# Kernel tuning notes

Measured on AMD Instinct MI355X. Metric: run time of the kernel, lower is better.

## Reference

```python
import jax, jax.numpy as jnp
import numpy as np

N = 100000      # num nodes
E = 1000000     # num directed edges
D_IN = 128      # input feature dim
D_H = 32        # hidden dim


def setup_inputs() -> dict:
    key = jax.random.key(0)
    ks = jax.random.split(key, 10)
    feat = jax.random.normal(ks[0], (N, D_IN), jnp.float32)
    src = jax.random.randint(ks[1], (E,), 0, N, dtype=jnp.int64)
    dst = jax.random.randint(ks[2], (E,), 0, N, dtype=jnp.int64)

    def lin(k, fan_in, fan_out):
        bound = 1.0 / np.sqrt(fan_in)
        kw, kb = jax.random.split(k)
        W = jax.random.uniform(kw, (fan_in, fan_out), jnp.float32, -bound, bound)
        b = jax.random.uniform(kb, (fan_out,), jnp.float32, -bound, bound)
        return W, b

    W_in, b_in = lin(ks[3], D_IN, D_H)        # input_project
    W_nbr, b_nbr = lin(ks[4], D_H, D_H)       # W_neighbor1 (Linear incl. its own bias)
    b_neighbor1 = jnp.zeros((D_H,), jnp.float32)  # extra learned bias, zero-init
    W_ffnn, b_ffnn = lin(ks[5], 2 * D_H, D_H)
    return {"feat": feat, "src": src, "dst": dst,
            "W_in": W_in, "b_in": b_in,
            "W_nbr": W_nbr, "b_nbr": b_nbr, "b_neighbor1": b_neighbor1,
            "W_ffnn": W_ffnn, "b_ffnn": b_ffnn}


def reference(feat, src, dst, W_in, b_in, W_nbr, b_nbr, b_neighbor1, W_ffnn, b_ffnn):
    # h = input_project(feat)  (input_dim != hidden_dim)
    h = feat @ W_in + b_in                                   # [N, D_H]

    # neighbors of v = predecessors (src where dst==v) + successors (dst where src==v)
    seg = jnp.concatenate([dst, src])                        # [2E] receiving node
    nbr = jnp.concatenate([src, dst])                        # [2E] neighbor node

    # sigmoid(W_neighbor1(h[nbr]) + b_neighbor1), then per-node max-pool
    t = jax.nn.sigmoid(h[nbr] @ W_nbr + b_nbr + b_neighbor1)  # [2E, D_H]
    agg = jax.ops.segment_max(t, seg, num_segments=N)         # [N, D_H]

    # nodes with total neighbor count <= 1 get zeros (faithful to `if len > 1`)
    deg = jax.ops.segment_sum(jnp.ones_like(seg, dtype=jnp.int32), seg, num_segments=N)
    agg = jnp.where((deg > 1)[:, None], agg, jnp.zeros((), jnp.float32))

    # concat + final linear
    out = jnp.concatenate([h, agg], axis=1) @ W_ffnn + b_ffnn  # [N, D_H]
    return out
```

## Files before the change

kernel.cpp:

```cpp
#include <hip/hip_runtime.h>
#include <hip/hip_bf16.h>

#define DH 32
#define BSZ 128
#define NBP 1024
#define SCAT_E 3840
#define SCAT_P (2 * SCAT_E)
#define EPT 15
#define PRE_E 8192
#define CPG 16
#define TS 4096
#define PAD 17
#define TPW 2

typedef short bf16x8 __attribute__((ext_vector_type(8)));
typedef float f32x4 __attribute__((ext_vector_type(4)));

__device__ __forceinline__ unsigned short f2bf(float x) {
    unsigned b = __float_as_uint(x);
    b += 0x7FFFu + ((b >> 16) & 1u);
    return (unsigned short)(b >> 16);
}

__global__ __launch_bounds__(256) void pre2(
    const int* __restrict__ src, const int* __restrict__ dst,
    int* __restrict__ gtotal, int E, int pgrid,
    const float* __restrict__ W_in, const float* __restrict__ W_nbr,
    const float* __restrict__ W_ffnn, unsigned short* __restrict__ wbf)
{
    __shared__ int hist[NBP];
    const int tid = threadIdx.x;

    if ((int)blockIdx.x == pgrid) {
        for (int i = tid; i < 4096; i += 256) {
            int c = i >> 7, k = i & 127;
            wbf[i] = f2bf(W_in[k * 32 + c]);
        }
        for (int i = tid; i < 1024; i += 256) {
            int c = i >> 5, k = i & 31;
            wbf[4096 + i] = f2bf(W_nbr[k * 32 + c]);
            wbf[5120 + i] = f2bf(W_ffnn[k * 32 + c]);
        }
        return;
    }

    for (int i = tid; i < NBP; i += 256) hist[i] = 0;
    __syncthreads();
    const int e0 = blockIdx.x * PRE_E;
    const int eend = min(e0 + PRE_E, E);
    for (int e = e0 + tid; e < eend; e += 256) {
        atomicAdd(&hist[src[e] >> 7], 1);
        atomicAdd(&hist[dst[e] >> 7], 1);
    }
    __syncthreads();
    for (int i = tid; i < NBP; i += 256)
        if (hist[i] > 0) atomicAdd(&gtotal[i], hist[i]);
}

__global__ __launch_bounds__(256) void scan_buckets(
    const int* __restrict__ gtotal, int* __restrict__ gbase,
    int* __restrict__ gcursor)
{
    __shared__ int ss[256];
    const int t = threadIdx.x;
    int v0 = gtotal[4 * t], v1 = gtotal[4 * t + 1];
    int v2 = gtotal[4 * t + 2], v3 = gtotal[4 * t + 3];
    int tsum = v0 + v1 + v2 + v3;
    ss[t] = tsum;
    __syncthreads();
    for (int off = 1; off < 256; off <<= 1) {
        int y = (t >= off) ? ss[t - off] : 0;
        __syncthreads();
        ss[t] += y;
        __syncthreads();
    }
    int e = ss[t] - tsum;
    gbase[4 * t] = e;                    gcursor[4 * t] = e;
    gbase[4 * t + 1] = e + v0;           gcursor[4 * t + 1] = e + v0;
    gbase[4 * t + 2] = e + v0 + v1;      gcursor[4 * t + 2] = e + v0 + v1;
    gbase[4 * t + 3] = e + v0 + v1 + v2; gcursor[4 * t + 3] = e + v0 + v1 + v2;
}

union SPSmem {
    struct {
        unsigned code[SCAT_P];
        int cur[NBP];
        int gbL[NBP];
    } sc;
    struct {
        unsigned short htile[4][16 * 32];
    } pj;
};

__global__ __launch_bounds__(256) void scatproj(
    const int* __restrict__ src, const int* __restrict__ dst,
    int* __restrict__ gcursor, unsigned* __restrict__ pairs_g,
    int E, int B, int egrid,
    const float* __restrict__ feat,
    const unsigned short* __restrict__ wbf,
    const float* __restrict__ b_in, const float* __restrict__ b_nbr,
    const float* __restrict__ b_n1, const float* __restrict__ b_ffnn,
    float* __restrict__ hpart, unsigned short* __restrict__ ub16,
    int N, int ntiles)
{
    __shared__ SPSmem sm;
    const int tid = threadIdx.x;

    if ((int)blockIdx.x < egrid) {
        const int e0 = blockIdx.x * SCAT_E;
        const int eend = min(e0 + SCAT_E, E);
        const int np = 2 * (eend - e0);

        for (int i = tid; i < NBP; i += 256) sm.sc.cur[i] = 0;
        __syncthreads();

        int es[EPT], dr[EPT];
#pragma unroll
        for (int j = 0; j < EPT; ++j) {
            int e = e0 + tid + j * 256;
            bool ok = (e < eend);
            es[j] = ok ? src[e] : -1;
            dr[j] = ok ? dst[e] : -1;
        }
#pragma unroll
        for (int j = 0; j < EPT; ++j) {
            if (es[j] >= 0) {
                atomicAdd(&sm.sc.cur[es[j] >> 7], 1);
                atomicAdd(&sm.sc.cur[dr[j] >> 7], 1);
            }
        }
        __syncthreads();

        {
            const int lane = tid & 63;
            const int w = tid >> 6;
            int v0 = sm.sc.cur[4 * tid], v1 = sm.sc.cur[4 * tid + 1];
            int v2 = sm.sc.cur[4 * tid + 2], v3 = sm.sc.cur[4 * tid + 3];
            int tsum = v0 + v1 + v2 + v3;
            int x = tsum;
#pragma unroll
            for (int off = 1; off < 64; off <<= 1) {
                int y = __shfl_up(x, off, 64);
                x += (lane >= off) ? y : 0;
            }
            if (lane == 63) sm.sc.gbL[w] = x;
            __syncthreads();
            int woff = 0;
#pragma unroll
            for (int k = 0; k < 4; ++k) woff += (k < w) ? sm.sc.gbL[k] : 0;
            int ebase = woff + x - tsum;
            __syncthreads();
            sm.sc.cur[4 * tid] = ebase;
            sm.sc.cur[4 * tid + 1] = ebase + v0;
            sm.sc.cur[4 * tid + 2] = ebase + v0 + v1;
            sm.sc.cur[4 * tid + 3] = ebase + v0 + v1 + v2;
        }
        __syncthreads();

#pragma unroll
        for (int j = 0; j < EPT; ++j) {
            if (es[j] >= 0) {
                int s = es[j], d = dr[j];
                int bs = s >> 7, bd = d >> 7;
                unsigned cs = ((unsigned)(bs & 255) << 24) |
                              ((unsigned)(s & 127) << 17) | (unsigned)d;
                unsigned cd = ((unsigned)(bd & 255) << 24) |
                              ((unsigned)(d & 127) << 17) | (unsigned)s;
                int p1 = atomicAdd(&sm.sc.cur[bs], 1);
                sm.sc.code[p1] = cs;
                int p2 = atomicAdd(&sm.sc.cur[bd], 1);
                sm.sc.code[p2] = cd;
            }
        }
        __syncthreads();

        for (int b = tid; b < B; b += 256) {
            int end = sm.sc.cur[b];
            int start = b ? sm.sc.cur[b - 1] : 0;
            int c = end - start;
            if (c > 0) {
                int gw = atomicAdd(&gcursor[b], c);
                sm.sc.gbL[b] = gw - start;
            }
        }
        __syncthreads();

        for (int i = tid; i < np; i += 256) {
            unsigned code = sm.sc.code[i];
            int cc = (int)(code >> 24);
#pragma unroll
            for (int k = 0; k < 3; ++k) {
                int hi2 = sm.sc.cur[cc];
                int lo2 = cc ? sm.sc.cur[cc - 1] : 0;
                bool in = (i < hi2) && (i >= lo2);
                cc = in ? cc : cc + 256;
            }
            pairs_g[sm.sc.gbL[cc] + i] = code & 0x00FFFFFFu;
        }
        return;
    }

    const int wid = tid >> 6, lane = tid & 63;
    const int r16 = lane & 15, kg = lane >> 4;
    const int w = ((int)blockIdx.x - egrid) * 4 + wid;
    const int t0 = w * TPW;
    if (t0 >= ntiles) return;

    const unsigned short* W1t = wbf;
    const unsigned short* W2t = wbf + 4096;
    const unsigned short* Wft = wbf + 5120;

    bf16x8 B1[4][2], B2[2], Bf[2];
#pragma unroll
    for (int ks = 0; ks < 4; ++ks)
#pragma unroll
        for (int ct = 0; ct < 2; ++ct)
            B1[ks][ct] = *(const bf16x8*)&W1t[(ct * 16 + r16) * 128 + ks * 32 + kg * 8];
#pragma unroll
    for (int ct = 0; ct < 2; ++ct) {
        B2[ct] = *(const bf16x8*)&W2t[(ct * 16 + r16) * 32 + kg * 8];
        Bf[ct] = *(const bf16x8*)&Wft[(ct * 16 + r16) * 32 + kg * 8];
    }

    const float b1a = b_in[r16],            b1b = b_in[16 + r16];
    const float b2a = b_nbr[r16] + b_n1[r16];
    const float b2b = b_nbr[16 + r16] + b_n1[16 + r16];
    const float bfa = b_ffnn[r16],          bfb = b_ffnn[16 + r16];

    unsigned short* hl = &sm.pj.htile[wid][0];

#pragma unroll
    for (int i = 0; i < TPW; ++i) {
        const int ti = t0 + i;
        const bool tv = (ti < ntiles);
        const int t = tv ? ti : ntiles - 1;
        const int tbase = t * 16;
        const int nA = tbase + r16;
        const bool okA = tv && (nA < N);
        const float* fr = feat + (size_t)(okA ? nA : 0) * 128;

        bf16x8 A[4];
#pragma unroll
        for (int ks = 0; ks < 4; ++ks) {
            float4 p0 = make_float4(0.f, 0.f, 0.f, 0.f);
            float4 p1 = make_float4(0.f, 0.f, 0.f, 0.f);
            if (okA) {
                p0 = *(const float4*)(fr + ks * 32 + kg * 8);
                p1 = *(const float4*)(fr + ks * 32 + kg * 8 + 4);
            }
            A[ks][0] = (short)f2bf(p0.x); A[ks][1] = (short)f2bf(p0.y);
            A[ks][2] = (short)f2bf(p0.z); A[ks][3] = (short)f2bf(p0.w);
            A[ks][4] = (short)f2bf(p1.x); A[ks][5] = (short)f2bf(p1.y);
            A[ks][6] = (short)f2bf(p1.z); A[ks][7] = (short)f2bf(p1.w);
        }

        f32x4 acc0 = {b1a, b1a, b1a, b1a};
        f32x4 acc1 = {b1b, b1b, b1b, b1b};
#pragma unroll
        for (int ks = 0; ks < 4; ++ks) {
            acc0 = __builtin_amdgcn_mfma_f32_16x16x32_bf16(A[ks], B1[ks][0], acc0, 0, 0, 0);
            acc1 = __builtin_amdgcn_mfma_f32_16x16x32_bf16(A[ks], B1[ks][1], acc1, 0, 0, 0);
        }

#pragma unroll
        for (int r = 0; r < 4; ++r) {
            hl[(kg * 4 + r) * 32 + r16]      = f2bf(acc0[r]);
            hl[(kg * 4 + r) * 32 + 16 + r16] = f2bf(acc1[r]);
        }
        asm volatile("s_waitcnt lgkmcnt(0)" ::: "memory");
        bf16x8 A2 = *reinterpret_cast<const bf16x8*>(&hl[r16 * 32 + kg * 8]);

        f32x4 u0 = {b2a, b2a, b2a, b2a};
        f32x4 u1 = {b2b, b2b, b2b, b2b};
        u0 = __builtin_amdgcn_mfma_f32_16x16x32_bf16(A2, B2[0], u0, 0, 0, 0);
        u1 = __builtin_amdgcn_mfma_f32_16x16x32_bf16(A2, B2[1], u1, 0, 0, 0);
        f32x4 g0 = {bfa, bfa, bfa, bfa};
        f32x4 g1 = {bfb, bfb, bfb, bfb};
        g0 = __builtin_amdgcn_mfma_f32_16x16x32_bf16(A2, Bf[0], g0, 0, 0, 0);
        g1 = __builtin_amdgcn_mfma_f32_16x16x32_bf16(A2, Bf[1], g1, 0, 0, 0);

#pragma unroll
        for (int r = 0; r < 4; ++r) {
            const int n2 = tbase + kg * 4 + r;
            if (tv && n2 < N) {
                float s0 = 1.0f / (1.0f + __expf(-u0[r]));
                float s1 = 1.0f / (1.0f + __expf(-u1[r]));
                ub16[(size_t)n2 * 16 + r16]       = f2bf(s0);
                ub16[((size_t)N + n2) * 16 + r16] = f2bf(s1);
                hpart[(size_t)n2 * 32 + r16]      = g0[r];
                hpart[(size_t)n2 * 32 + 16 + r16] = g1[r];
            }
        }
    }
}

__global__ __launch_bounds__(256) void bucket_max(
    const unsigned* __restrict__ pairs_g, const int* __restrict__ gbase,
    const int* __restrict__ gtotal, const unsigned* __restrict__ ub32,
    float* __restrict__ agg, int N, int B)
{
    __shared__ unsigned aggL[BSZ * PAD];
    __shared__ int degL[BSZ];
    __shared__ unsigned tile[TS];

    const int tid = threadIdx.x;
    const int bid = blockIdx.x;
    const int xcd = bid & 7;
    const int q = xcd >> 2;
    const int b = (bid >> 3) * 4 + (xcd & 3);
    if (b >= B) return;
    const int v0 = b * BSZ;
    const unsigned* ut = ub32 + (size_t)q * N * 8;

    for (int i = tid; i < BSZ * PAD; i += 256) aggL[i] = 0u;
    for (int i = tid; i < BSZ; i += 256) degL[i] = 0;
    __syncthreads();

    const int start = gbase[b];
    const int cnt = gtotal[b];
    const int gg = tid >> 3;
    const int cl = tid & 7;

    for (int t0 = 0; t0 < cnt; t0 += TS) {
        const int tn = min(TS, cnt - t0);
        for (int i = tid; i < tn; i += 256) tile[i] = pairs_g[start + t0 + i];
        __syncthreads();

        const int kmax = (tn - gg + 31) >> 5;
        const int pm = tn - 1;
        for (int kk = 0; kk < kmax; kk += 16) {
            unsigned cc[16], xx[16];
#pragma unroll
            for (int u = 0; u < 16; ++u)
                cc[u] = tile[min(gg + (kk + u) * 32, pm)];
#pragma unroll
            for (int u = 0; u < 16; ++u)
                xx[u] = ut[(size_t)(cc[u] & 0x1FFFF) * 8 + cl];
#pragma unroll
            for (int u = 0; u < 16; ++u) {
                atomicMax(&aggL[(cc[u] >> 17) * PAD + 2 * cl], (xx[u] & 0xFFFFu) << 16);
                atomicMax(&aggL[(cc[u] >> 17) * PAD + 2 * cl + 1], xx[u] & 0xFFFF0000u);
            }
            if (cl == 0) {
#pragma unroll
                for (int u = 0; u < 16; ++u)
                    if (gg + (kk + u) * 32 < tn) atomicAdd(&degL[cc[u] >> 17], 1);
            }
        }
        __syncthreads();
    }

    for (int i = tid; i < BSZ * CPG; i += 256) {
        int vl = i >> 4;
        int v = v0 + vl;
        if (v < N) {
            float val = (degL[vl] > 1) ? __uint_as_float(aggL[vl * PAD + (i & 15)]) : 0.f;
            agg[(size_t)v * DH + q * CPG + (i & 15)] = val;
        }
    }
}

__global__ __launch_bounds__(256) void fin(
    const float* __restrict__ hpart, const float* __restrict__ agg,
    const float* __restrict__ W_ffnn, float* __restrict__ out, int N)
{
    const int node = blockIdx.x * 256 + threadIdx.x;
    if (node >= N) return;

    const float4* hr = (const float4*)(hpart + (size_t)node * 32);
    const float4* ar = (const float4*)(agg + (size_t)node * 32);

    float acc[32], a[32];
#pragma unroll
    for (int c4 = 0; c4 < 8; ++c4) {
        float4 v = hr[c4];
        acc[c4 * 4 + 0] = v.x; acc[c4 * 4 + 1] = v.y;
        acc[c4 * 4 + 2] = v.z; acc[c4 * 4 + 3] = v.w;
        float4 w = ar[c4];
        a[c4 * 4 + 0] = w.x; a[c4 * 4 + 1] = w.y;
        a[c4 * 4 + 2] = w.z; a[c4 * 4 + 3] = w.w;
    }

    const float* W2h = W_ffnn + 1024;
#pragma unroll
    for (int k = 0; k < 32; ++k) {
        const float hv = a[k];
        const float* wr = W2h + k * 32;
#pragma unroll
        for (int c = 0; c < 32; ++c)
            acc[c] = fmaf(hv, wr[c], acc[c]);
    }

    float4* orow = (float4*)(out + (size_t)node * 32);
#pragma unroll
    for (int c4 = 0; c4 < 8; ++c4)
        orow[c4] = make_float4(acc[c4 * 4 + 0], acc[c4 * 4 + 1],
                               acc[c4 * 4 + 2], acc[c4 * 4 + 3]);
}

extern "C" void kernel_launch(void* const* d_in, const int* in_sizes, int n_in,
                              void* d_out, int out_size, void* d_ws, size_t ws_size,
                              hipStream_t stream)
{
    const float* feat   = (const float*)d_in[0];
    const int*   src    = (const int*)d_in[1];
    const int*   dst    = (const int*)d_in[2];
    const float* W_in   = (const float*)d_in[3];
    const float* b_in   = (const float*)d_in[4];
    const float* W_nbr  = (const float*)d_in[5];
    const float* b_nbr  = (const float*)d_in[6];
    const float* b_n1   = (const float*)d_in[7];
    const float* W_ffnn = (const float*)d_in[8];
    const float* b_ffnn = (const float*)d_in[9];
    float* out = (float*)d_out;

    const int N = in_sizes[0] / 128;
    const int E = in_sizes[1];
    const int B = (N + BSZ - 1) / BSZ;
    const int ntiles = (N + 15) / 16;

    unsigned short* ub16 = (unsigned short*)out;
    float* hpart   = (float*)d_ws;
    float* agg     = hpart + (size_t)N * DH;
    int*   gtotal  = (int*)(agg + (size_t)N * DH);
    int*   gbase   = gtotal + NBP;
    int*   gcursor = gbase + NBP;
    unsigned* pairs_g = (unsigned*)(gcursor + NBP);
    unsigned short* wbf = (unsigned short*)(pairs_g + 2 * (size_t)E);

    const int egrid = (E + SCAT_E - 1) / SCAT_E;
    const int pgrid = (E + PRE_E - 1) / PRE_E;
    const int jgrid = (ntiles + 4 * TPW - 1) / (4 * TPW);
    const int npb = (N + 255) / 256;

    hipMemsetAsync(gtotal, 0, NBP * sizeof(int), stream);
    pre2<<<pgrid + 1, 256, 0, stream>>>(src, dst, gtotal, E, pgrid,
                                        W_in, W_nbr, W_ffnn, wbf);
    scan_buckets<<<1, 256, 0, stream>>>(gtotal, gbase, gcursor);
    scatproj<<<egrid + jgrid, 256, 0, stream>>>(
        src, dst, gcursor, pairs_g, E, B, egrid,
        feat, wbf, b_in, b_nbr, b_n1, b_ffnn,
        hpart, ub16, N, ntiles);
    bucket_max<<<((B + 3) / 4) * 8, 256, 0, stream>>>(
        pairs_g, gbase, gtotal, (const unsigned*)ub16, agg, N, B);
    fin<<<npb, 256, 0, stream>>>(hpart, agg, W_ffnn, out, N);
}
```

Baseline: 105.7 us.

## Fuse bucket max-pool with final linear layer, one block per bucket

Merges the bucket_max and fin kernels into one kernel. Each 512-thread block now handles all 32 feature channels of a 128-node bucket instead of splitting channels into two halves across blocks, and applies the second half of W_ffnn directly from shared memory. The sigmoid table moves to node-interleaved layout (32 bf16 per node) in workspace, and the agg intermediate buffer and one launch are removed. In exchange, each edge gather now fetches 64 bytes per neighbor instead of 32, the XCD-aware block mapping is dropped, and per-block work doubles, which halves the block count.

```diff
diff --git a/kernel.cpp b/kernel.cpp
--- a/kernel.cpp
+++ b/kernel.cpp
@@ -8,9 +8,8 @@
 #define SCAT_P (2 * SCAT_E)
 #define EPT 15
 #define PRE_E 8192
-#define CPG 16
 #define TS 4096
-#define PAD 17
+#define PAD2 33
 #define TPW 2
 
 typedef short bf16x8 __attribute__((ext_vector_type(8)));
@@ -285,8 +284,8 @@
             if (tv && n2 < N) {
                 float s0 = 1.0f / (1.0f + __expf(-u0[r]));
                 float s1 = 1.0f / (1.0f + __expf(-u1[r]));
-                ub16[(size_t)n2 * 16 + r16]       = f2bf(s0);
-                ub16[((size_t)N + n2) * 16 + r16] = f2bf(s1);
+                ub16[(size_t)n2 * 32 + r16]       = f2bf(s0);
+                ub16[(size_t)n2 * 32 + 16 + r16]  = f2bf(s1);
                 hpart[(size_t)n2 * 32 + r16]      = g0[r];
                 hpart[(size_t)n2 * 32 + 16 + r16] = g1[r];
             }
@@ -294,36 +293,34 @@
     }
 }
 
-__global__ __launch_bounds__(256) void bucket_max(
+__global__ __launch_bounds__(512) void bmaxfin(
     const unsigned* __restrict__ pairs_g, const int* __restrict__ gbase,
-    const int* __restrict__ gtotal, const unsigned* __restrict__ ub32,
-    float* __restrict__ agg, int N, int B)
+    const int* __restrict__ gtotal, const unsigned* __restrict__ ut32,
+    const float* __restrict__ hpart, const float* __restrict__ W_ffnn,
+    float* __restrict__ out, int N, int B)
 {
-    __shared__ unsigned aggL[BSZ * PAD];
+    __shared__ unsigned aggL[BSZ * PAD2];
     __shared__ int degL[BSZ];
     __shared__ unsigned tile[TS];
+    __shared__ float sWf[1024];
 
     const int tid = threadIdx.x;
-    const int bid = blockIdx.x;
-    const int xcd = bid & 7;
-    const int q = xcd >> 2;
-    const int b = (bid >> 3) * 4 + (xcd & 3);
-    if (b >= B) return;
+    const int b = blockIdx.x;
     const int v0 = b * BSZ;
-    const unsigned* ut = ub32 + (size_t)q * N * 8;
-
-    for (int i = tid; i < BSZ * PAD; i += 256) aggL[i] = 0u;
-    for (int i = tid; i < BSZ; i += 256) degL[i] = 0;
+
+    for (int i = tid; i < BSZ * PAD2; i += 512) aggL[i] = 0u;
+    for (int i = tid; i < BSZ; i += 512) degL[i] = 0;
+    for (int i = tid; i < 1024; i += 512) sWf[i] = W_ffnn[1024 + i];
     __syncthreads();
 
     const int start = gbase[b];
     const int cnt = gtotal[b];
-    const int gg = tid >> 3;
-    const int cl = tid & 7;
+    const int gg = tid >> 4;
+    const int cl = tid & 15;
 
     for (int t0 = 0; t0 < cnt; t0 += TS) {
         const int tn = min(TS, cnt - t0);
-        for (int i = tid; i < tn; i += 256) tile[i] = pairs_g[start + t0 + i];
+        for (int i = tid; i < tn; i += 512) tile[i] = pairs_g[start + t0 + i];
         __syncthreads();
 
         const int kmax = (tn - gg + 31) >> 5;
@@ -335,11 +332,11 @@
                 cc[u] = tile[min(gg + (kk + u) * 32, pm)];
 #pragma unroll
             for (int u = 0; u < 16; ++u)
-                xx[u] = ut[(size_t)(cc[u] & 0x1FFFF) * 8 + cl];
+                xx[u] = ut32[(size_t)(cc[u] & 0x1FFFF) * 16 + cl];
 #pragma unroll
             for (int u = 0; u < 16; ++u) {
-                atomicMax(&aggL[(cc[u] >> 17) * PAD + 2 * cl], (xx[u] & 0xFFFFu) << 16);
-                atomicMax(&aggL[(cc[u] >> 17) * PAD + 2 * cl + 1], xx[u] & 0xFFFF0000u);
+                atomicMax(&aggL[(cc[u] >> 17) * PAD2 + 2 * cl], (xx[u] & 0xFFFFu) << 16);
+                atomicMax(&aggL[(cc[u] >> 17) * PAD2 + 2 * cl + 1], xx[u] & 0xFFFF0000u);
             }
             if (cl == 0) {
 #pragma unroll
@@ -350,52 +347,29 @@
         __syncthreads();
     }
 
-    for (int i = tid; i < BSZ * CPG; i += 256) {
-        int vl = i >> 4;
-        int v = v0 + vl;
-        if (v < N) {
-            float val = (degL[vl] > 1) ? __uint_as_float(aggL[vl * PAD + (i & 15)]) : 0.f;
-            agg[(size_t)v * DH + q * CPG + (i & 15)] = val;
-        }
-    }
-}
-
-__global__ __launch_bounds__(256) void fin(
-    const float* __restrict__ hpart, const float* __restrict__ agg,
-    const float* __restrict__ W_ffnn, float* __restrict__ out, int N)
-{
-    const int node = blockIdx.x * 256 + threadIdx.x;
-    if (node >= N) return;
-
-    const float4* hr = (const float4*)(hpart + (size_t)node * 32);
-    const float4* ar = (const float4*)(agg + (size_t)node * 32);
-
-    float acc[32], a[32];
-#pragma unroll
-    for (int c4 = 0; c4 < 8; ++c4) {
-        float4 v = hr[c4];
-        acc[c4 * 4 + 0] = v.x; acc[c4 * 4 + 1] = v.y;
-        acc[c4 * 4 + 2] = v.z; acc[c4 * 4 + 3] = v.w;
-        float4 w = ar[c4];
-        a[c4 * 4 + 0] = w.x; a[c4 * 4 + 1] = w.y;
-        a[c4 * 4 + 2] = w.z; a[c4 * 4 + 3] = w.w;
-    }
-
-    const float* W2h = W_ffnn + 1024;
-#pragma unroll
-    for (int k = 0; k < 32; ++k) {
-        const float hv = a[k];
-        const float* wr = W2h + k * 32;
-#pragma unroll
-        for (int c = 0; c < 32; ++c)
-            acc[c] = fmaf(hv, wr[c], acc[c]);
-    }
-
-    float4* orow = (float4*)(out + (size_t)node * 32);
-#pragma unroll
-    for (int c4 = 0; c4 < 8; ++c4)
-        orow[c4] = make_float4(acc[c4 * 4 + 0], acc[c4 * 4 + 1],
-                               acc[c4 * 4 + 2], acc[c4 * 4 + 3]);
+    const int vl = tid >> 2;
+    const int c0 = (tid & 3) * 8;
+    const int v = v0 + vl;
+    if (v < N) {
+        float acc[8];
+        const float4* hr = (const float4*)(hpart + (size_t)v * 32 + c0);
+        float4 h0 = hr[0], h1 = hr[1];
+        acc[0] = h0.x; acc[1] = h0.y; acc[2] = h0.z; acc[3] = h0.w;
+        acc[4] = h1.x; acc[5] = h1.y; acc[6] = h1.z; acc[7] = h1.w;
+        if (degL[vl] > 1) {
+#pragma unroll
+            for (int k = 0; k < 32; ++k) {
+                float av = __uint_as_float(aggL[vl * PAD2 + k]);
+                const float* wr = &sWf[k * 32 + c0];
+#pragma unroll
+                for (int j = 0; j < 8; ++j)
+                    acc[j] = fmaf(av, wr[j], acc[j]);
+            }
+        }
+        float4* orow = (float4*)(out + (size_t)v * 32 + c0);
+        orow[0] = make_float4(acc[0], acc[1], acc[2], acc[3]);
+        orow[1] = make_float4(acc[4], acc[5], acc[6], acc[7]);
+    }
 }
 
 extern "C" void kernel_launch(void* const* d_in, const int* in_sizes, int n_in,
@@ -419,10 +393,9 @@
     const int B = (N + BSZ - 1) / BSZ;
     const int ntiles = (N + 15) / 16;
 
-    unsigned short* ub16 = (unsigned short*)out;
     float* hpart   = (float*)d_ws;
-    float* agg     = hpart + (size_t)N * DH;
-    int*   gtotal  = (int*)(agg + (size_t)N * DH);
+    unsigned short* ub16 = (unsigned short*)(hpart + (size_t)N * DH);
+    int*   gtotal  = (int*)(ub16 + (size_t)N * DH);
     int*   gbase   = gtotal + NBP;
     int*   gcursor = gbase + NBP;
     unsigned* pairs_g = (unsigned*)(gcursor + NBP);
@@ -431,7 +404,6 @@
     const int egrid = (E + SCAT_E - 1) / SCAT_E;
     const int pgrid = (E + PRE_E - 1) / PRE_E;
     const int jgrid = (ntiles + 4 * TPW - 1) / (4 * TPW);
-    const int npb = (N + 255) / 256;
 
     hipMemsetAsync(gtotal, 0, NBP * sizeof(int), stream);
     pre2<<<pgrid + 1, 256, 0, stream>>>(src, dst, gtotal, E, pgrid,
@@ -441,7 +413,7 @@
         src, dst, gcursor, pairs_g, E, B, egrid,
         feat, wbf, b_in, b_nbr, b_n1, b_ffnn,
         hpart, ub16, N, ntiles);
-    bucket_max<<<((B + 3) / 4) * 8, 256, 0, stream>>>(
-        pairs_g, gbase, gtotal, (const unsigned*)ub16, agg, N, B);
-    fin<<<npb, 256, 0, stream>>>(hpart, agg, W_ffnn, out, N);
-}
+    bmaxfin<<<B, 512, 0, stream>>>(
+        pairs_g, gbase, gtotal, (const unsigned*)ub16, hpart, W_ffnn,
+        out, N, B);
+}
```

After: 90.54 us, median of 3. 14.4% less time.
